# Optimization experiments

Hardware: AMD Instinct MI355X
Metric: run time of the kernel (lower is better)

## Reference

```python
import jax, jax.numpy as jnp
import numpy as np

H = 12          # num_attention_heads
D = 64          # attention_head_size
HID = H * D     # hidden_size = 768
M = 1024        # max_position_embeddings


def setup_inputs() -> dict:
    key = jax.random.key(0)
    ks = jax.random.split(key, 9)
    B, S = 4, 1024
    s = 0.02
    return {
        "hidden_states": jax.random.normal(ks[0], (B, S, HID), jnp.float32),
        "attention_mask": jnp.zeros((B, 1, 1, S), jnp.float32),
        "Wq": jax.random.normal(ks[1], (HID, HID), jnp.float32) * s,
        "bq": jnp.zeros((HID,), jnp.float32),
        "Wk": jax.random.normal(ks[2], (HID, HID), jnp.float32) * s,
        "bk": jnp.zeros((HID,), jnp.float32),
        "Wv": jax.random.normal(ks[3], (HID, HID), jnp.float32) * s,
        "bv": jnp.zeros((HID,), jnp.float32),
        "dist_emb": jax.random.normal(ks[4], (2 * M - 1, D), jnp.float32) * s,
    }


def reference(hidden_states, attention_mask, Wq, bq, Wk, bk, Wv, bv, dist_emb):
    B, S, _ = hidden_states.shape

    def heads(x):  # [B,S,HID] -> [B,H,S,D]
        return x.reshape(B, S, H, D).transpose(0, 2, 1, 3)

    q = heads(hidden_states @ Wq + bq)
    k = heads(hidden_states @ Wk + bk)
    v = heads(hidden_states @ Wv + bv)

    # raw dot-product scores [B,H,S,S]
    scores = jnp.einsum('bhld,bhrd->bhlr', q, k)

    # relative_key_query positional bias
    pos = jnp.arange(S)
    distance = pos[:, None] - pos[None, :] + (M - 1)   # [S,S] in [0, 2M-2]
    pe = dist_emb[distance]                            # [S,S,D]
    scores = scores + jnp.einsum('bhld,lrd->bhlr', q, pe) \
                    + jnp.einsum('bhrd,lrd->bhlr', k, pe)

    scores = scores / jnp.sqrt(jnp.asarray(D, scores.dtype)) + attention_mask
    probs = jax.nn.softmax(scores, axis=-1)            # dropout is identity in eval

    ctx = jnp.einsum('bhlr,bhrd->bhld', probs, v)      # [B,H,S,D]
    ctx = ctx.transpose(0, 2, 1, 3).reshape(B, S, HID)
    return ctx, probs
```

## Files before the change

kernel.cpp:

```cpp
#include <hip/hip_runtime.h>
#include <hip/hip_bf16.h>

#define DEVFN __device__ __forceinline__

typedef __bf16 bf16x8 __attribute__((ext_vector_type(8)));
typedef float f32x4 __attribute__((ext_vector_type(4)));
typedef unsigned short ushort8 __attribute__((ext_vector_type(8)));
typedef unsigned short us4 __attribute__((ext_vector_type(4)));

namespace {

constexpr int S = 1024;
constexpr int HID = 768;
constexpr int NH = 12;
constexpr int HD = 64;

DEVFN unsigned short f2bf(float f) {
  union { float f; unsigned u; } v; v.f = f;
  unsigned r = v.u + 0x7FFF + ((v.u >> 16) & 1);
  return (unsigned short)(r >> 16);
}

DEVFN float bf2f(unsigned short u) {
  union { unsigned u; float f; } v; v.u = ((unsigned)u) << 16; return v.f;
}

DEVFN f32x4 zero4() { return f32x4{0.f, 0.f, 0.f, 0.f}; }

DEVFN f32x4 mfma_bf16(bf16x8 a, bf16x8 b, f32x4 c) {
  return __builtin_amdgcn_mfma_f32_16x16x32_bf16(a, b, c, 0, 0, 0);
}

DEVFN void gload16(void* lds_base, const void* gsrc) {
  __builtin_amdgcn_global_load_lds(
      (const __attribute__((address_space(1))) void*)gsrc,
      (__attribute__((address_space(3))) void*)lds_base, 16, 0, 0);
}

DEVFN bf16x8 frag_ld(const char* tile, int row, int ch) {
  int chs = ch ^ (row & 7);
  return *(const bf16x8*)(tile + row * 128 + chs * 16);
}

__global__ void k0_cvt_x(const float* __restrict__ x, unsigned short* __restrict__ xb) {
  size_t i = (size_t)(blockIdx.x * 256 + threadIdx.x) * 8;
  float4 a = *(const float4*)(x + i);
  float4 c = *(const float4*)(x + i + 4);
  ushort8 o;
  o[0] = f2bf(a.x); o[1] = f2bf(a.y); o[2] = f2bf(a.z); o[3] = f2bf(a.w);
  o[4] = f2bf(c.x); o[5] = f2bf(c.y); o[6] = f2bf(c.z); o[7] = f2bf(c.w);
  *(ushort8*)(xb + i) = o;
}

__global__ void k0_cvt_pe(const float* __restrict__ de, unsigned short* __restrict__ peb) {
  size_t i = (size_t)(blockIdx.x * 256 + threadIdx.x) * 8;
  int row = (int)(i >> 6);
  ushort8 o;
  if (row < 2047) {
    float4 a = *(const float4*)(de + i);
    float4 c = *(const float4*)(de + i + 4);
    o[0] = f2bf(a.x); o[1] = f2bf(a.y); o[2] = f2bf(a.z); o[3] = f2bf(a.w);
    o[4] = f2bf(c.x); o[5] = f2bf(c.y); o[6] = f2bf(c.z); o[7] = f2bf(c.w);
  } else {
    o = ushort8{0, 0, 0, 0, 0, 0, 0, 0};
  }
  *(ushort8*)(peb + i) = o;
}

__global__ __launch_bounds__(256) void k0_wt(const float* __restrict__ Wq,
                                             const float* __restrict__ Wk,
                                             const float* __restrict__ Wv,
                                             unsigned short* __restrict__ wt) {
  __shared__ float t[64][65];
  int bidx = blockIdx.x;
  int sec = bidx / 144, rem = bidx % 144;
  int ktb = rem / 12, ntb = rem % 12;
  const float* W = (sec == 0) ? Wq : ((sec == 1) ? Wk : Wv);
  int k0 = ktb * 64, n0 = ntb * 64;
  int tid = threadIdx.x;
  #pragma unroll
  for (int p = 0; p < 4; ++p) {
    int id = p * 256 + tid;
    int row = id >> 4, ch = id & 15;
    float4 v = *(const float4*)(W + (size_t)(k0 + row) * 768 + n0 + ch * 4);
    t[row][ch * 4 + 0] = v.x; t[row][ch * 4 + 1] = v.y;
    t[row][ch * 4 + 2] = v.z; t[row][ch * 4 + 3] = v.w;
  }
  __syncthreads();
  #pragma unroll
  for (int p = 0; p < 2; ++p) {
    int id = p * 256 + tid;
    int nrow = id >> 3, c8 = id & 7;
    ushort8 o;
    #pragma unroll
    for (int i = 0; i < 8; ++i) o[i] = f2bf(t[c8 * 8 + i][nrow]);
    *(ushort8*)(wt + (size_t)(sec * 768 + n0 + nrow) * 768 + k0 + c8 * 8) = o;
  }
}

__global__ __launch_bounds__(256) void k1_qkv(
    const unsigned short* __restrict__ xb, const unsigned short* __restrict__ wt,
    const float* __restrict__ bq, const float* __restrict__ bk, const float* __restrict__ bv,
    unsigned short* __restrict__ q_ws, unsigned short* __restrict__ k_ws,
    unsigned short* __restrict__ vt_ws) {
  __shared__ char ldsA[8192], ldsB[8192];
  const int tid = threadIdx.x, lane = tid & 63, wv = tid >> 6;
  const int row16 = lane & 15, cgrp = lane >> 4;
  const int ntb = blockIdx.x % 36, mtb = blockIdx.x / 36;
  const int sec = ntb / 12;
  const int n0 = ntb * 64;
  const int m0 = mtb * 64;

  f32x4 acc[4] = {zero4(), zero4(), zero4(), zero4()};

  for (int k0 = 0; k0 < 768; k0 += 64) {
    #pragma unroll
    for (int c = 0; c < 2; ++c) {
      int cc = (wv * 2 + c) * 64 + lane;
      int row = cc >> 3, ch = cc & 7, chs = ch ^ (row & 7);
      gload16(ldsA + (wv * 2 + c) * 1024, xb + (size_t)(m0 + row) * 768 + k0 + chs * 8);
      gload16(ldsB + (wv * 2 + c) * 1024, wt + (size_t)(n0 + row) * 768 + k0 + chs * 8);
    }
    __syncthreads();
    if (sec < 2) {
      bf16x8 af[2];
      #pragma unroll
      for (int k2 = 0; k2 < 2; ++k2) af[k2] = frag_ld(ldsA, wv * 16 + row16, k2 * 4 + cgrp);
      #pragma unroll
      for (int nt = 0; nt < 4; ++nt)
        #pragma unroll
        for (int k2 = 0; k2 < 2; ++k2) {
          bf16x8 bf = frag_ld(ldsB, nt * 16 + row16, k2 * 4 + cgrp);
          acc[nt] = mfma_bf16(af[k2], bf, acc[nt]);
        }
    } else {
      bf16x8 af[2];
      #pragma unroll
      for (int k2 = 0; k2 < 2; ++k2) af[k2] = frag_ld(ldsB, wv * 16 + row16, k2 * 4 + cgrp);
      #pragma unroll
      for (int mt = 0; mt < 4; ++mt)
        #pragma unroll
        for (int k2 = 0; k2 < 2; ++k2) {
          bf16x8 bx = frag_ld(ldsA, mt * 16 + row16, k2 * 4 + cgrp);
          acc[mt] = mfma_bf16(af[k2], bx, acc[mt]);
        }
    }
    __syncthreads();
  }

  if (sec < 2) {
    unsigned short* dst = (sec == 0) ? q_ws : k_ws;
    const float* bias = (sec == 0) ? bq : bk;
    int nl0 = (ntb % 12) * 64;
    #pragma unroll
    for (int nt = 0; nt < 4; ++nt) {
      int nn = nl0 + nt * 16 + row16;
      float bb = bias[nn];
      int hh = nn >> 6, dd = nn & 63;
      #pragma unroll
      for (int j = 0; j < 4; ++j) {
        int m = m0 + wv * 16 + cgrp * 4 + j;
        int b_ = m >> 10, s_ = m & 1023;
        dst[(size_t)((b_ * 12 + hh) * 1024 + s_) * 64 + dd] = f2bf(acc[nt][j] + bb);
      }
    }
  } else {
    int nl0 = (ntb % 12) * 64;
    #pragma unroll
    for (int j = 0; j < 4; ++j) {
      int nn = nl0 + wv * 16 + cgrp * 4 + j;
      float bb = bv[nn];
      int hh = nn >> 6, dd = nn & 63;
      #pragma unroll
      for (int mt = 0; mt < 4; ++mt) {
        int m = m0 + mt * 16 + row16;
        int b_ = m >> 10, s_ = m & 1023;
        vt_ws[(size_t)((b_ * 12 + hh) * 64 + dd) * 1024 + s_] = f2bf(acc[mt][j] + bb);
      }
    }
  }
}

__global__ __launch_bounds__(256) void kA_attn(
    const unsigned short* __restrict__ q_ws, const unsigned short* __restrict__ k_ws,
    const unsigned short* __restrict__ vt_ws, const unsigned short* __restrict__ peb,
    const float* __restrict__ mask, float* __restrict__ out_ctx,
    float* __restrict__ out_probs) {
  __shared__ unsigned short p_lds[32 * 1024];
  __shared__ unsigned short s3t[4][48 * 36];
  __shared__ float rsp[32][2];

  const int tid = threadIdx.x, lane = tid & 63, wv = tid >> 6;
  const int wl = wv >> 1, wr = wv & 1;
  const int row16 = lane & 15, cgrp = lane >> 4;

  const int qt = blockIdx.x & 31, bh = blockIdx.x >> 5;
  const int b = bh / NH, h = bh % NH;
  const int l0 = qt * 32;

  const unsigned short* qh = q_ws + (size_t)bh * S * HD;
  const unsigned short* khp = k_ws + (size_t)bh * S * HD;
  const unsigned short* vth = vt_ws + (size_t)bh * HD * S;
  const float* maskb = mask + b * S;

  bf16x8 qf[2];
  #pragma unroll
  for (int k2 = 0; k2 < 2; ++k2)
    qf[k2] = *(const bf16x8*)(qh + (size_t)(l0 + wl * 16 + row16) * HD + k2 * 32 + cgrp * 8);

  unsigned short* s3w = &s3t[wv][0];
  float rs[4] = {0.f, 0.f, 0.f, 0.f};

  for (int rt = 0; rt < 16; ++rt) {
    const int rbase = rt * 64 + wr * 32;

    bf16x8 kf[2][2];
    #pragma unroll
    for (int rtl = 0; rtl < 2; ++rtl)
      #pragma unroll
      for (int k2 = 0; k2 < 2; ++k2)
        kf[rtl][k2] = *(const bf16x8*)(khp + (size_t)(rbase + rtl * 16 + row16) * HD +
                                       k2 * 32 + cgrp * 8);

    const int pe_base = l0 + wl * 16 - rbase + 992;
    bf16x8 pef[3][2];
    #pragma unroll
    for (int jt = 0; jt < 3; ++jt)
      #pragma unroll
      for (int k2 = 0; k2 < 2; ++k2)
        pef[jt][k2] = *(const bf16x8*)(peb + (size_t)(pe_base + jt * 16 + row16) * HD +
                                       k2 * 32 + cgrp * 8);

    #pragma unroll
    for (int rtl = 0; rtl < 2; ++rtl)
      #pragma unroll
      for (int jt = 0; jt < 3; ++jt) {
        f32x4 a3 = zero4();
        a3 = mfma_bf16(kf[rtl][0], pef[jt][0], a3);
        a3 = mfma_bf16(kf[rtl][1], pef[jt][1], a3);
        us4 o;
        o[0] = f2bf(a3[0]); o[1] = f2bf(a3[1]); o[2] = f2bf(a3[2]); o[3] = f2bf(a3[3]);
        *(us4*)(s3w + (jt * 16 + row16) * 36 + rtl * 16 + cgrp * 4) = o;
      }

    f32x4 s1[2];
    #pragma unroll
    for (int rtl = 0; rtl < 2; ++rtl) {
      f32x4 a = zero4();
      a = mfma_bf16(qf[0], kf[rtl][0], a);
      a = mfma_bf16(qf[1], kf[rtl][1], a);
      s1[rtl] = a;
    }
    f32x4 s2[3];
    #pragma unroll
    for (int jt = 0; jt < 3; ++jt) {
      f32x4 a = zero4();
      a = mfma_bf16(qf[0], pef[jt][0], a);
      a = mfma_bf16(qf[1], pef[jt][1], a);
      s2[jt] = a;
    }

    #pragma unroll
    for (int rtl = 0; rtl < 2; ++rtl) {
      float mval = maskb[rbase + rtl * 16 + row16];
      const int jtA = 1 - rtl;
      #pragma unroll
      for (int j = 0; j < 4; ++j) {
        int dl = cgrp * 4 + j;
        int dr = rtl * 16 + row16;
        int jjq = dl - dr + 31;
        int src = (lane & 48) | (jjq & 15);
        float vA = __shfl(s2[jtA][j], src, 64);
        float vB = __shfl(s2[jtA + 1][j], src, 64);
        float b1 = ((jjq >> 4) == jtA) ? vA : vB;
        float b2 = bf2f(s3w[jjq * 36 + dr]);
        float logit = (s1[rtl][j] + b1 + b2) * 0.125f + mval;
        float p = __expf(logit);
        rs[j] += p;
        int prow = wl * 16 + dl;
        int pcol = rbase + dr;
        int chs = (pcol >> 3) ^ (prow & 7);
        p_lds[prow * 1024 + chs * 8 + (pcol & 7)] = f2bf(p);
      }
    }
  }

  #pragma unroll
  for (int j = 0; j < 4; ++j) {
    float v = rs[j];
    v += __shfl_xor(v, 1, 64);
    v += __shfl_xor(v, 2, 64);
    v += __shfl_xor(v, 4, 64);
    v += __shfl_xor(v, 8, 64);
    if (row16 == 0) rsp[wl * 16 + cgrp * 4 + j][wr] = v;
  }
  __syncthreads();

  f32x4 ctxacc[2] = {zero4(), zero4()};
  {
    const int prow = wl * 16 + row16;
    for (int ks = 0; ks < 32; ++ks) {
      int chs = (ks * 4 + cgrp) ^ (prow & 7);
      bf16x8 pa = *(const bf16x8*)(p_lds + prow * 1024 + chs * 8);
      #pragma unroll
      for (int dt = 0; dt < 2; ++dt) {
        bf16x8 vb = *(const bf16x8*)(vth + (size_t)(wr * 32 + dt * 16 + row16) * S +
                                     ks * 32 + cgrp * 8);
        ctxacc[dt] = mfma_bf16(pa, vb, ctxacc[dt]);
      }
    }
  }
  #pragma unroll
  for (int dt = 0; dt < 2; ++dt)
    #pragma unroll
    for (int j = 0; j < 4; ++j) {
      int lr = wl * 16 + cgrp * 4 + j;
      float iv = 1.0f / (rsp[lr][0] + rsp[lr][1]);
      out_ctx[((size_t)(b * S + l0 + lr)) * HID + h * HD + wr * 32 + dt * 16 + row16] =
          ctxacc[dt][j] * iv;
    }

  {
    const int wrow0 = tid >> 5;
    const int c32 = tid & 31;
    float* probs_bh = out_probs + (size_t)bh * S * S;
    #pragma unroll
    for (int rp = 0; rp < 4; ++rp) {
      int row = rp * 8 + wrow0;
      float iv = 1.0f / (rsp[row][0] + rsp[row][1]);
      float* dst = probs_bh + (size_t)(l0 + row) * S;
      #pragma unroll
      for (int cc = 0; cc < 4; ++cc) {
        int ch = cc * 32 + c32;
        int chs = ch ^ (row & 7);
        ushort8 w = *(const ushort8*)(p_lds + row * 1024 + chs * 8);
        float4 lo{bf2f(w[0]) * iv, bf2f(w[1]) * iv, bf2f(w[2]) * iv, bf2f(w[3]) * iv};
        float4 hi{bf2f(w[4]) * iv, bf2f(w[5]) * iv, bf2f(w[6]) * iv, bf2f(w[7]) * iv};
        *(float4*)(dst + ch * 8) = lo;
        *(float4*)(dst + ch * 8 + 4) = hi;
      }
    }
  }
}

}

extern "C" void kernel_launch(void* const* d_in, const int* in_sizes, int n_in,
                              void* d_out, int out_size, void* d_ws, size_t ws_size,
                              hipStream_t stream) {
  const float* hidden = (const float*)d_in[0];
  const float* mask   = (const float*)d_in[1];
  const float* Wq = (const float*)d_in[2];
  const float* bq = (const float*)d_in[3];
  const float* Wk = (const float*)d_in[4];
  const float* bk = (const float*)d_in[5];
  const float* Wv = (const float*)d_in[6];
  const float* bv = (const float*)d_in[7];
  const float* de = (const float*)d_in[8];

  unsigned short* ws = (unsigned short*)d_ws;
  unsigned short* q_ws  = ws;
  unsigned short* k_ws  = ws + 3145728;
  unsigned short* vt_ws = ws + 6291456;
  unsigned short* xb    = ws + 9437184;
  unsigned short* wt    = ws + 12582912;
  unsigned short* peb   = ws + 14352384;

  float* outc = (float*)d_out;
  float* outp = outc + (size_t)4 * 1024 * 768;

  hipLaunchKernelGGL(k0_cvt_x, dim3(1536), dim3(256), 0, stream, hidden, xb);
  hipLaunchKernelGGL(k0_cvt_pe, dim3(64), dim3(256), 0, stream, de, peb);
  hipLaunchKernelGGL(k0_wt, dim3(432), dim3(256), 0, stream, Wq, Wk, Wv, wt);
  hipLaunchKernelGGL(k1_qkv, dim3(2304), dim3(256), 0, stream,
                     xb, wt, bq, bk, bv, q_ws, k_ws, vt_ws);
  hipLaunchKernelGGL(kA_attn, dim3(1536), dim3(256), 0, stream,
                     q_ws, k_ws, vt_ws, peb, mask, outc, outp);
}
```

Baseline: 219.0 us.

## Restructure attention kernel to 16-row query tiles with software-pipelined K/PE loads

The attention kernel now gives each block 16 query rows instead of 32, which doubles the grid and halves the LDS probability buffer so more blocks can be resident per CU. Each wave handles its own 16-key slice, and both relative-position bias terms now go through LDS tiles instead of cross-lane shuffles. K and position-embedding loads are double-buffered so global loads overlap the MFMA work. Block indices are swizzled across heads for locality. The cost is that K/V/PE reuse per block halves, so total global traffic rises.

```diff
diff --git a/kernel.cpp b/kernel.cpp
--- a/kernel.cpp
+++ b/kernel.cpp
@@ -181,22 +181,23 @@
   }
 }
 
-__global__ __launch_bounds__(256) void kA_attn(
+__global__ __launch_bounds__(256) void kB_attn(
     const unsigned short* __restrict__ q_ws, const unsigned short* __restrict__ k_ws,
     const unsigned short* __restrict__ vt_ws, const unsigned short* __restrict__ peb,
     const float* __restrict__ mask, float* __restrict__ out_ctx,
     float* __restrict__ out_probs) {
-  __shared__ unsigned short p_lds[32 * 1024];
-  __shared__ unsigned short s3t[4][48 * 36];
-  __shared__ float rsp[32][2];
+  __shared__ __align__(16) unsigned short p_lds[16 * 1024];
+  __shared__ __align__(16) unsigned short s3t[4][16 * 36];
+  __shared__ __align__(16) unsigned short s2t[4][16 * 36];
+  __shared__ __align__(16) float rsp[16][4];
 
   const int tid = threadIdx.x, lane = tid & 63, wv = tid >> 6;
-  const int wl = wv >> 1, wr = wv & 1;
   const int row16 = lane & 15, cgrp = lane >> 4;
 
-  const int qt = blockIdx.x & 31, bh = blockIdx.x >> 5;
+  const int swz = (blockIdx.x & 7) * 384 + (blockIdx.x >> 3);
+  const int qt = swz & 63, bh = swz >> 6;
   const int b = bh / NH, h = bh % NH;
-  const int l0 = qt * 32;
+  const int l0 = qt * 16;
 
   const unsigned short* qh = q_ws + (size_t)bh * S * HD;
   const unsigned short* khp = k_ws + (size_t)bh * S * HD;
@@ -206,139 +207,123 @@
   bf16x8 qf[2];
   #pragma unroll
   for (int k2 = 0; k2 < 2; ++k2)
-    qf[k2] = *(const bf16x8*)(qh + (size_t)(l0 + wl * 16 + row16) * HD + k2 * 32 + cgrp * 8);
+    qf[k2] = *(const bf16x8*)(qh + (size_t)(l0 + row16) * HD + k2 * 32 + cgrp * 8);
 
   unsigned short* s3w = &s3t[wv][0];
-  float rs[4] = {0.f, 0.f, 0.f, 0.f};
-
-  for (int rt = 0; rt < 16; ++rt) {
-    const int rbase = rt * 64 + wr * 32;
-
-    bf16x8 kf[2][2];
-    #pragma unroll
-    for (int rtl = 0; rtl < 2; ++rtl)
+  unsigned short* s2w = &s2t[wv][0];
+  float rs = 0.f;
+  const int xsw = 2 * row16;
+
+  auto loadK = [&](int rbase, bf16x8 (&kf)[2]) {
+    #pragma unroll
+    for (int k2 = 0; k2 < 2; ++k2)
+      kf[k2] = *(const bf16x8*)(khp + (size_t)(rbase + row16) * HD + k2 * 32 + cgrp * 8);
+  };
+  auto loadPE = [&](int rbase, bf16x8 (&pef)[2][2]) {
+    int pe0 = l0 - rbase + 1008;
+    #pragma unroll
+    for (int jt = 0; jt < 2; ++jt)
       #pragma unroll
       for (int k2 = 0; k2 < 2; ++k2)
-        kf[rtl][k2] = *(const bf16x8*)(khp + (size_t)(rbase + rtl * 16 + row16) * HD +
+        pef[jt][k2] = *(const bf16x8*)(peb + (size_t)(pe0 + jt * 16 + row16) * HD +
                                        k2 * 32 + cgrp * 8);
-
-    const int pe_base = l0 + wl * 16 - rbase + 992;
-    bf16x8 pef[3][2];
-    #pragma unroll
-    for (int jt = 0; jt < 3; ++jt)
-      #pragma unroll
-      for (int k2 = 0; k2 < 2; ++k2)
-        pef[jt][k2] = *(const bf16x8*)(peb + (size_t)(pe_base + jt * 16 + row16) * HD +
-                                       k2 * 32 + cgrp * 8);
-
-    #pragma unroll
-    for (int rtl = 0; rtl < 2; ++rtl)
-      #pragma unroll
-      for (int jt = 0; jt < 3; ++jt) {
-        f32x4 a3 = zero4();
-        a3 = mfma_bf16(kf[rtl][0], pef[jt][0], a3);
-        a3 = mfma_bf16(kf[rtl][1], pef[jt][1], a3);
-        us4 o;
-        o[0] = f2bf(a3[0]); o[1] = f2bf(a3[1]); o[2] = f2bf(a3[2]); o[3] = f2bf(a3[3]);
-        *(us4*)(s3w + (jt * 16 + row16) * 36 + rtl * 16 + cgrp * 4) = o;
-      }
-
-    f32x4 s1[2];
-    #pragma unroll
-    for (int rtl = 0; rtl < 2; ++rtl) {
+  };
+  auto compute = [&](int rbase, const bf16x8 (&kf)[2], const bf16x8 (&pef)[2][2]) {
+    #pragma unroll
+    for (int jt = 0; jt < 2; ++jt) {
       f32x4 a = zero4();
-      a = mfma_bf16(qf[0], kf[rtl][0], a);
-      a = mfma_bf16(qf[1], kf[rtl][1], a);
-      s1[rtl] = a;
-    }
-    f32x4 s2[3];
-    #pragma unroll
-    for (int jt = 0; jt < 3; ++jt) {
+      a = mfma_bf16(pef[jt][0], kf[0], a);
+      a = mfma_bf16(pef[jt][1], kf[1], a);
+      us4 o;
+      o[0] = f2bf(a[0]); o[1] = f2bf(a[1]); o[2] = f2bf(a[2]); o[3] = f2bf(a[3]);
+      *(us4*)(s3w + row16 * 36 + jt * 16 + cgrp * 4) = o;
+    }
+    #pragma unroll
+    for (int jt = 0; jt < 2; ++jt) {
       f32x4 a = zero4();
-      a = mfma_bf16(qf[0], pef[jt][0], a);
-      a = mfma_bf16(qf[1], pef[jt][1], a);
-      s2[jt] = a;
-    }
-
-    #pragma unroll
-    for (int rtl = 0; rtl < 2; ++rtl) {
-      float mval = maskb[rbase + rtl * 16 + row16];
-      const int jtA = 1 - rtl;
-      #pragma unroll
-      for (int j = 0; j < 4; ++j) {
-        int dl = cgrp * 4 + j;
-        int dr = rtl * 16 + row16;
-        int jjq = dl - dr + 31;
-        int src = (lane & 48) | (jjq & 15);
-        float vA = __shfl(s2[jtA][j], src, 64);
-        float vB = __shfl(s2[jtA + 1][j], src, 64);
-        float b1 = ((jjq >> 4) == jtA) ? vA : vB;
-        float b2 = bf2f(s3w[jjq * 36 + dr]);
-        float logit = (s1[rtl][j] + b1 + b2) * 0.125f + mval;
-        float p = __expf(logit);
-        rs[j] += p;
-        int prow = wl * 16 + dl;
-        int pcol = rbase + dr;
-        int chs = (pcol >> 3) ^ (prow & 7);
-        p_lds[prow * 1024 + chs * 8 + (pcol & 7)] = f2bf(p);
-      }
-    }
-  }
+      a = mfma_bf16(pef[jt][0], qf[0], a);
+      a = mfma_bf16(pef[jt][1], qf[1], a);
+      us4 o;
+      o[0] = f2bf(a[0]); o[1] = f2bf(a[1]); o[2] = f2bf(a[2]); o[3] = f2bf(a[3]);
+      *(us4*)(s2w + row16 * 36 + jt * 16 + cgrp * 4) = o;
+    }
+    f32x4 s1 = zero4();
+    s1 = mfma_bf16(kf[0], qf[0], s1);
+    s1 = mfma_bf16(kf[1], qf[1], s1);
+
+    float4 mv = *(const float4*)(maskb + rbase + cgrp * 4);
+    const float* mvp = (const float*)&mv;
+    float pv[4];
+    #pragma unroll
+    for (int j = 0; j < 4; ++j) {
+      int rl = cgrp * 4 + j;
+      int jj = row16 - rl + 15;
+      float b1 = bf2f(s2w[row16 * 36 + jj]);
+      float b2 = bf2f(s3w[rl * 36 + jj]);
+      float logit = (s1[j] + b1 + b2) * 0.125f + mvp[j];
+      pv[j] = __expf(logit);
+      rs += pv[j];
+    }
+    unsigned lo = (unsigned)f2bf(pv[0]) | ((unsigned)f2bf(pv[1]) << 16);
+    unsigned hi = (unsigned)f2bf(pv[2]) | ((unsigned)f2bf(pv[3]) << 16);
+    int c8 = (rbase >> 2) + cgrp;
+    *(uint2*)((char*)p_lds + row16 * 2048 + (size_t)((c8 ^ xsw) * 8)) = uint2{lo, hi};
+  };
+
+  bf16x8 kfA[2], kfB[2], peA[2][2], peB[2][2];
+  const int rb0 = wv * 16;
+  loadK(rb0, kfA); loadPE(rb0, peA);
+  #pragma unroll 1
+  for (int rt2 = 0; rt2 < 8; ++rt2) {
+    const int ra = rt2 * 128 + rb0;
+    loadK(ra + 64, kfB); loadPE(ra + 64, peB);
+    compute(ra, kfA, peA);
+    if (rt2 < 7) { loadK(ra + 128, kfA); loadPE(ra + 128, peA); }
+    compute(ra + 64, kfB, peB);
+  }
+
+  rs += __shfl_xor(rs, 16, 64);
+  rs += __shfl_xor(rs, 32, 64);
+  if (lane < 16) rsp[lane][wv] = rs;
+  __syncthreads();
+
+  f32x4 ctx0 = zero4(), ctx1 = zero4();
+  #pragma unroll 4
+  for (int ks = 0; ks < 32; ks += 2) {
+    int c8a = ks * 8 + cgrp * 2;
+    bf16x8 pa0 = *(const bf16x8*)((char*)p_lds + row16 * 2048 + (size_t)((c8a ^ xsw) * 8));
+    bf16x8 pa1 = *(const bf16x8*)((char*)p_lds + row16 * 2048 +
+                                  (size_t)(((c8a + 8) ^ xsw) * 8));
+    bf16x8 vb0 = *(const bf16x8*)(vth + (size_t)(wv * 16 + row16) * S + ks * 32 + cgrp * 8);
+    bf16x8 vb1 = *(const bf16x8*)(vth + (size_t)(wv * 16 + row16) * S + ks * 32 + 32 + cgrp * 8);
+    ctx0 = mfma_bf16(pa0, vb0, ctx0);
+    ctx1 = mfma_bf16(pa1, vb1, ctx1);
+  }
+  ctx0[0] += ctx1[0]; ctx0[1] += ctx1[1]; ctx0[2] += ctx1[2]; ctx0[3] += ctx1[3];
 
   #pragma unroll
   for (int j = 0; j < 4; ++j) {
-    float v = rs[j];
-    v += __shfl_xor(v, 1, 64);
-    v += __shfl_xor(v, 2, 64);
-    v += __shfl_xor(v, 4, 64);
-    v += __shfl_xor(v, 8, 64);
-    if (row16 == 0) rsp[wl * 16 + cgrp * 4 + j][wr] = v;
-  }
-  __syncthreads();
-
-  f32x4 ctxacc[2] = {zero4(), zero4()};
+    int l = cgrp * 4 + j;
+    float4 r4 = *(const float4*)&rsp[l][0];
+    float iv = 1.0f / (r4.x + r4.y + r4.z + r4.w);
+    out_ctx[((size_t)(b * S + l0 + l)) * HID + h * HD + wv * 16 + row16] = ctx0[j] * iv;
+  }
+
   {
-    const int prow = wl * 16 + row16;
-    for (int ks = 0; ks < 32; ++ks) {
-      int chs = (ks * 4 + cgrp) ^ (prow & 7);
-      bf16x8 pa = *(const bf16x8*)(p_lds + prow * 1024 + chs * 8);
-      #pragma unroll
-      for (int dt = 0; dt < 2; ++dt) {
-        bf16x8 vb = *(const bf16x8*)(vth + (size_t)(wr * 32 + dt * 16 + row16) * S +
-                                     ks * 32 + cgrp * 8);
-        ctxacc[dt] = mfma_bf16(pa, vb, ctxacc[dt]);
-      }
-    }
-  }
-  #pragma unroll
-  for (int dt = 0; dt < 2; ++dt)
-    #pragma unroll
-    for (int j = 0; j < 4; ++j) {
-      int lr = wl * 16 + cgrp * 4 + j;
-      float iv = 1.0f / (rsp[lr][0] + rsp[lr][1]);
-      out_ctx[((size_t)(b * S + l0 + lr)) * HID + h * HD + wr * 32 + dt * 16 + row16] =
-          ctxacc[dt][j] * iv;
-    }
-
-  {
-    const int wrow0 = tid >> 5;
-    const int c32 = tid & 31;
-    float* probs_bh = out_probs + (size_t)bh * S * S;
-    #pragma unroll
-    for (int rp = 0; rp < 4; ++rp) {
-      int row = rp * 8 + wrow0;
-      float iv = 1.0f / (rsp[row][0] + rsp[row][1]);
-      float* dst = probs_bh + (size_t)(l0 + row) * S;
-      #pragma unroll
-      for (int cc = 0; cc < 4; ++cc) {
-        int ch = cc * 32 + c32;
-        int chs = ch ^ (row & 7);
-        ushort8 w = *(const ushort8*)(p_lds + row * 1024 + chs * 8);
-        float4 lo{bf2f(w[0]) * iv, bf2f(w[1]) * iv, bf2f(w[2]) * iv, bf2f(w[3]) * iv};
-        float4 hi{bf2f(w[4]) * iv, bf2f(w[5]) * iv, bf2f(w[6]) * iv, bf2f(w[7]) * iv};
-        *(float4*)(dst + ch * 8) = lo;
-        *(float4*)(dst + ch * 8 + 4) = hi;
-      }
+    const int prow = tid >> 4, t = tid & 15;
+    float4 r4 = *(const float4*)&rsp[prow][0];
+    const float iv = 1.0f / (r4.x + r4.y + r4.z + r4.w);
+    float* dst = out_probs + ((size_t)bh * S + l0 + prow) * S;
+    const int xsr = 2 * prow;
+    #pragma unroll
+    for (int seg = 0; seg < 8; ++seg) {
+      int cc = seg * 16 + t;
+      ushort8 w = *(const ushort8*)((char*)p_lds + prow * 2048 +
+                                    (size_t)((((cc * 2) ^ xsr)) * 8));
+      float4 lo{bf2f(w[0]) * iv, bf2f(w[1]) * iv, bf2f(w[2]) * iv, bf2f(w[3]) * iv};
+      float4 hi{bf2f(w[4]) * iv, bf2f(w[5]) * iv, bf2f(w[6]) * iv, bf2f(w[7]) * iv};
+      *(float4*)(dst + cc * 8) = lo;
+      *(float4*)(dst + cc * 8 + 4) = hi;
     }
   }
 }
@@ -374,6 +359,6 @@
   hipLaunchKernelGGL(k0_wt, dim3(432), dim3(256), 0, stream, Wq, Wk, Wv, wt);
   hipLaunchKernelGGL(k1_qkv, dim3(2304), dim3(256), 0, stream,
                      xb, wt, bq, bk, bv, q_ws, k_ws, vt_ws);
-  hipLaunchKernelGGL(kA_attn, dim3(1536), dim3(256), 0, stream,
+  hipLaunchKernelGGL(kB_attn, dim3(3072), dim3(256), 0, stream,
                      q_ws, k_ws, vt_ws, peb, mask, outc, outp);
 }
```

After: 234.3 us. 7.0% more time.
